# Performance work log

Hardware: AMD Instinct MI355X
Metric: run time of the kernel (lower is better)

Reference implementation:

```python
import jax, jax.numpy as jnp
import numpy as np

B, S, H, NH = 2, 2048, 1024, 16
HD = H // NH  # 64
SCALE = HD ** -0.5


def setup_inputs() -> dict:
    key = jax.random.key(0)
    k1, k2, k3 = jax.random.split(key, 3)
    x = jax.random.normal(k1, (B, S, H), dtype=jnp.float32)
    w_qkv = jax.random.normal(k2, (H, 3 * H), dtype=jnp.float32) * (H ** -0.5)
    b_qkv = jnp.zeros((3 * H,), dtype=jnp.float32)
    w_out = jax.random.normal(k3, (H, H), dtype=jnp.float32) * (H ** -0.5)
    b_out = jnp.zeros((H,), dtype=jnp.float32)
    return {"x": x, "w_qkv": w_qkv, "b_qkv": b_qkv, "w_out": w_out, "b_out": b_out}


def reference(x, w_qkv, b_qkv, w_out, b_out):
    # qkv projection: [B,S,3H] -> split -> [B,NH,S,HD] each
    qkv = x @ w_qkv + b_qkv
    q, k, v = jnp.split(qkv, 3, axis=-1)
    def heads(t):
        return t.reshape(B, S, NH, HD).transpose(0, 2, 1, 3)  # [B,NH,S,HD]
    q, k, v = heads(q), heads(k), heads(v)
    # full (non-causal) softmax attention; chunking in the original is
    # math-equivalent since each query row attends over all keys
    scores = jnp.einsum('bhqd,bhkd->bhqk', q, k) * SCALE
    attn = jax.nn.softmax(scores, axis=-1)
    out = jnp.einsum('bhqk,bhkd->bhqd', attn, v)  # [B,NH,S,HD]
    out = out.transpose(0, 2, 1, 3).reshape(B, S, H)
    # to_out linear (Dropout is identity in eval mode)
    return out @ w_out + b_out
```

## Files before the change

### kernel.cpp

```cpp
#include <hip/hip_runtime.h>
#include <cstdint>

using u16 = unsigned short;
typedef __bf16 bf16x8 __attribute__((ext_vector_type(8)));
typedef __bf16 bf16x4 __attribute__((ext_vector_type(4)));
typedef __bf16 bf16x2 __attribute__((ext_vector_type(2)));
typedef float f32x4 __attribute__((ext_vector_type(4)));

#define MFMA16(a, b, c) __builtin_amdgcn_mfma_f32_16x16x32_bf16((a), (b), (c), 0, 0, 0)

__device__ __forceinline__ u16 f2bf(float f) {
  union { float f; uint32_t u; } c; c.f = f;
  uint32_t u = c.u;
  u += 0x7fffu + ((u >> 16) & 1u);
  return (u16)(u >> 16);
}

#if __has_builtin(__builtin_amdgcn_global_load_lds)
#define GLOAD_LDS16(g, l)                                                      \
  __builtin_amdgcn_global_load_lds(                                            \
      (__attribute__((address_space(1))) void*)(g),                            \
      (__attribute__((address_space(3))) void*)(l), 16, 0, 0)
#else
#define GLOAD_LDS16(g, l) do { *(uint4*)(l) = *(const uint4*)(g); } while (0)
#endif

__device__ __forceinline__ bf16x8 ptrans(const f32x4 lo, const f32x4 hi) {
  union W { bf16x2 h; uint32_t u; } wl0, wl1, wh0, wh1;
  wl0.h[0] = (__bf16)lo[0]; wl0.h[1] = (__bf16)lo[1];
  wl1.h[0] = (__bf16)lo[2]; wl1.h[1] = (__bf16)lo[3];
  wh0.h[0] = (__bf16)hi[0]; wh0.h[1] = (__bf16)hi[1];
  wh1.h[0] = (__bf16)hi[2]; wh1.h[1] = (__bf16)hi[3];
  uint32_t a0 = wl0.u, b0 = wh0.u, a1 = wl1.u, b1 = wh1.u;
  asm("v_permlane32_swap_b32 %0, %1" : "+v"(a0), "+v"(b0));
  asm("v_permlane16_swap_b32 %0, %1" : "+v"(a0), "+v"(b0));
  asm("v_permlane32_swap_b32 %0, %1" : "+v"(a1), "+v"(b1));
  asm("v_permlane16_swap_b32 %0, %1" : "+v"(a1), "+v"(b1));
  union R { uint32_t u[4]; bf16x8 v; } r;
  r.u[0] = a0; r.u[1] = a1; r.u[2] = b0; r.u[3] = b1;
  return r.v;
}

__global__ __launch_bounds__(256) void prep(
    const float* __restrict__ x, const float* __restrict__ w_qkv,
    const float* __restrict__ w_out, u16* __restrict__ xb,
    u16* __restrict__ wqT, u16* __restrict__ woT) {
  const int bid = blockIdx.x, tid = threadIdx.x;
  if (bid < 4096) {
    int i = (bid * 256 + tid) * 4;
    float4 v = *(const float4*)&x[i];
    ushort4 p;
    p.x = f2bf(v.x); p.y = f2bf(v.y); p.z = f2bf(v.z); p.w = f2bf(v.w);
    *(ushort4*)&xb[i] = p;
    return;
  }
  __shared__ float tile[32][33];
  int t = bid - 4096;
  const float* in;
  u16* outp;
  int C, bx, by;
  if (t < 3072) { in = w_qkv; outp = wqT; C = 3072; bx = (t % 96) * 32; by = (t / 96) * 32; }
  else { t -= 3072; in = w_out; outp = woT; C = 1024; bx = (t % 32) * 32; by = (t / 32) * 32; }
  const int tx = tid & 31, ty = tid >> 5;
#pragma unroll
  for (int r2 = 0; r2 < 4; ++r2)
    tile[ty + r2 * 8][tx] = in[(size_t)(by + ty + r2 * 8) * C + bx + tx];
  __syncthreads();
#pragma unroll
  for (int r2 = 0; r2 < 4; ++r2)
    outp[(size_t)(bx + ty + r2 * 8) * 1024 + by + tx] = f2bf(tile[tx][ty + r2 * 8]);
}

__global__ __launch_bounds__(256, 3) void gemm_qkv(
    const u16* __restrict__ A, const u16* __restrict__ Bt,
    const float* __restrict__ bias,
    u16* __restrict__ qb, u16* __restrict__ kb, u16* __restrict__ vb,
    int M, int N, int K) {
  __shared__ u16 As[128 * 32];
  __shared__ u16 Bs[128 * 32];
  const int tid = threadIdx.x;
  const int m0 = blockIdx.x * 128;
  const int n0 = blockIdx.y * 128;
  const int lane = tid & 63, w = tid >> 6;
  const int quad = lane >> 4, l16 = lane & 15;
  const int wr = w >> 1, wc = w & 1;

  f32x4 acc[4][4] = {};

  const int r0 = tid >> 2, p0 = tid & 3;
  const int r1 = r0 + 64;
  const int c8 = p0 ^ ((r0 >> 1) & 3);
  const u16* ga0 = A + (size_t)(m0 + r0) * K + c8 * 8;
  const u16* ga1 = A + (size_t)(m0 + r1) * K + c8 * 8;
  const u16* gb0 = Bt + (size_t)(n0 + r0) * K + c8 * 8;
  const u16* gb1 = Bt + (size_t)(n0 + r1) * K + c8 * 8;
  u16* la0 = &As[tid * 8];
  u16* la1 = &As[(tid + 256) * 8];
  u16* lb0 = &Bs[tid * 8];
  u16* lb1 = &Bs[(tid + 256) * 8];

  int aoff[4], boff[4];
#pragma unroll
  for (int i = 0; i < 4; ++i) {
    int ra = wr * 64 + i * 16 + l16;
    aoff[i] = (ra * 4 + (quad ^ ((ra >> 1) & 3))) * 8;
    int rb = wc * 64 + i * 16 + l16;
    boff[i] = (rb * 4 + (quad ^ ((rb >> 1) & 3))) * 8;
  }

  const int nIter = K >> 5;
  for (int kt = 0; kt < nIter; ++kt) {
    __syncthreads();
    const int kk = kt << 5;
    GLOAD_LDS16(ga0 + kk, la0);
    GLOAD_LDS16(ga1 + kk, la1);
    GLOAD_LDS16(gb0 + kk, lb0);
    GLOAD_LDS16(gb1 + kk, lb1);
    __syncthreads();
    bf16x8 af[4], bfr[4];
#pragma unroll
    for (int i = 0; i < 4; ++i) af[i] = *(const bf16x8*)&As[aoff[i]];
#pragma unroll
    for (int j = 0; j < 4; ++j) bfr[j] = *(const bf16x8*)&Bs[boff[j]];
#pragma unroll
    for (int i = 0; i < 4; ++i)
#pragma unroll
      for (int j = 0; j < 4; ++j)
        acc[i][j] = MFMA16(af[i], bfr[j], acc[i][j]);
  }

  const int S = 2048, NH = 16;
#pragma unroll
  for (int i = 0; i < 4; ++i) {
    const int mb = m0 + wr * 64 + i * 16 + quad * 4;
#pragma unroll
    for (int j = 0; j < 4; ++j) {
      const int n = n0 + wc * 64 + j * 16 + l16;
      const float bv = bias[n];
      const int which = n >> 10;
      const int hn = n & 1023;
      const int h = hn >> 6, d = hn & 63;
      const int b = mb >> 11, s = mb & 2047;
      const int bh = b * NH + h;
      if (which == 2) {
        ushort4 pk;
        pk.x = f2bf(acc[i][j][0] + bv);
        pk.y = f2bf(acc[i][j][1] + bv);
        pk.z = f2bf(acc[i][j][2] + bv);
        pk.w = f2bf(acc[i][j][3] + bv);
        *(ushort4*)&vb[((size_t)bh * 64 + d) * S + s] = pk;
      } else {
        const float sc = (which == 0) ? 0.18033688f : 1.0f;
        u16* dst = (which == 0) ? qb : kb;
#pragma unroll
        for (int r = 0; r < 4; ++r)
          dst[((size_t)bh * S + s + r) * 64 + d] = f2bf((acc[i][j][r] + bv) * sc);
      }
    }
  }
}

__global__ __launch_bounds__(256, 2) void gemm_out(
    const u16* __restrict__ A, const u16* __restrict__ Bt,
    const float* __restrict__ bias, float* __restrict__ outf,
    int M, int N, int K) {
  __shared__ u16 As[64 * 32];
  __shared__ u16 Bs[128 * 32];
  const int tid = threadIdx.x;
  const int m0 = blockIdx.x * 64;
  const int n0 = blockIdx.y * 128;
  const int lane = tid & 63, w = tid >> 6;
  const int quad = lane >> 4, l16 = lane & 15;
  const int wr = w >> 1, wc = w & 1;

  f32x4 acc[2][4] = {};

  const int r0 = tid >> 2, p0 = tid & 3;
  const int c8 = p0 ^ ((r0 >> 1) & 3);
  const u16* ga0 = A + (size_t)(m0 + r0) * K + c8 * 8;
  const u16* gb0 = Bt + (size_t)(n0 + r0) * K + c8 * 8;
  const u16* gb1 = Bt + (size_t)(n0 + r0 + 64) * K + c8 * 8;
  u16* la0 = &As[tid * 8];
  u16* lb0 = &Bs[tid * 8];
  u16* lb1 = &Bs[(tid + 256) * 8];

  int aoff[2], boff[4];
#pragma unroll
  for (int i = 0; i < 2; ++i) {
    int ra = wr * 32 + i * 16 + l16;
    aoff[i] = (ra * 4 + (quad ^ ((ra >> 1) & 3))) * 8;
  }
#pragma unroll
  for (int j = 0; j < 4; ++j) {
    int rb = wc * 64 + j * 16 + l16;
    boff[j] = (rb * 4 + (quad ^ ((rb >> 1) & 3))) * 8;
  }

  const int nIter = K >> 5;
  for (int kt = 0; kt < nIter; ++kt) {
    __syncthreads();
    const int kk = kt << 5;
    GLOAD_LDS16(ga0 + kk, la0);
    GLOAD_LDS16(gb0 + kk, lb0);
    GLOAD_LDS16(gb1 + kk, lb1);
    __syncthreads();
    bf16x8 af[2], bfr[4];
#pragma unroll
    for (int i = 0; i < 2; ++i) af[i] = *(const bf16x8*)&As[aoff[i]];
#pragma unroll
    for (int j = 0; j < 4; ++j) bfr[j] = *(const bf16x8*)&Bs[boff[j]];
#pragma unroll
    for (int i = 0; i < 2; ++i)
#pragma unroll
      for (int j = 0; j < 4; ++j)
        acc[i][j] = MFMA16(af[i], bfr[j], acc[i][j]);
  }

#pragma unroll
  for (int i = 0; i < 2; ++i) {
    const int mb = m0 + wr * 32 + i * 16 + quad * 4;
#pragma unroll
    for (int j = 0; j < 4; ++j) {
      const int n = n0 + wc * 64 + j * 16 + l16;
      const float bv = bias[n];
#pragma unroll
      for (int r = 0; r < 4; ++r)
        outf[(size_t)(mb + r) * N + n] = acc[i][j][r] + bv;
    }
  }
}

__global__ __launch_bounds__(256, 2) void attn_fa(
    const u16* __restrict__ qg, const u16* __restrict__ kg,
    const u16* __restrict__ vg, u16* __restrict__ o) {
  const int S = 2048;
  const int lin = blockIdx.x;
  const int xcd = lin & 7, chunk = lin >> 3;
  const int bh = xcd * 4 + (chunk & 3);
  const int qblk = chunk >> 2;
  const int b = bh >> 4, h = bh & 15;
  const int tid = threadIdx.x, w = tid >> 6, lane = tid & 63;
  const int quad = lane >> 4, l16 = lane & 15;
  const int wq = w >> 1, wk = w & 1;

  __shared__ u16 Ks[2][8192];
  __shared__ u16 Vs[2][8192];

  const int q0w = qblk * 128 + wq * 64;
  bf16x8 qf[4][2];
#pragma unroll
  for (int qt = 0; qt < 4; ++qt)
#pragma unroll
    for (int dh = 0; dh < 2; ++dh)
      qf[qt][dh] = *(const bf16x8*)(qg + ((size_t)bh * S + q0w + qt * 16 + l16) * 64 +
                                    dh * 32 + quad * 8);

  f32x4 accO[4][4] = {};
  f32x4 accL[4] = {};

  bf16x8 ones;
#pragma unroll
  for (int i = 0; i < 8; ++i) ones[i] = (__bf16)1.0f;

  const u16* kbase = kg + (size_t)bh * S * 64;
  const u16* vbase = vg + (size_t)bh * 64 * S;

  const int sr0 = tid >> 3, sp0 = tid & 7;
  const int c8s = sp0 ^ (sr0 & 7);
  const u16* kSrc = kbase + (size_t)sr0 * 64 + c8s * 8;
  const u16* vSrc = vbase + (size_t)sr0 * S + c8s * 8;

  const int kgA = (quad ^ (l16 & 7)) * 8;
  const int kgB = ((quad + 4) ^ (l16 & 7)) * 8;

#define STAGE_KV(KT, NB)                                                      \
  {                                                                           \
    _Pragma("unroll")                                                         \
    for (int seg = 0; seg < 4; ++seg) {                                       \
      GLOAD_LDS16(kSrc + (size_t)((KT) * 128 + seg * 32) * 64,                \
                  &Ks[NB][(seg * 256 + tid) * 8]);                            \
      GLOAD_LDS16(vSrc + (size_t)(seg & 1) * 32 * S + (KT) * 128 +            \
                      (seg >> 1) * 64,                                        \
                  &Vs[NB][(seg * 256 + tid) * 8]);                            \
    }                                                                         \
  }

  STAGE_KV(0, 0);

  for (int kt = 0; kt < 16; ++kt) {
    const int cur = kt & 1;
    __syncthreads();
    const u16* Kc = Ks[cur];
    const u16* Vc = Vs[cur];

    bf16x8 kf[4][2];
#pragma unroll
    for (int ct = 0; ct < 4; ++ct) {
      const int rb = (wk * 64 + ct * 16 + l16) * 64;
      kf[ct][0] = *(const bf16x8*)&Kc[rb + kgA];
      kf[ct][1] = *(const bf16x8*)&Kc[rb + kgB];
    }

    if (kt + 1 < 16) STAGE_KV(kt + 1, cur ^ 1);

    f32x4 s[4][4] = {};
    __builtin_amdgcn_s_setprio(1);
#pragma unroll
    for (int ct = 0; ct < 4; ++ct)
#pragma unroll
      for (int qt = 0; qt < 4; ++qt) {
        s[ct][qt] = MFMA16(kf[ct][0], qf[qt][0], s[ct][qt]);
        s[ct][qt] = MFMA16(kf[ct][1], qf[qt][1], s[ct][qt]);
      }
    __builtin_amdgcn_s_setprio(0);

#pragma unroll
    for (int ct = 0; ct < 4; ++ct)
#pragma unroll
      for (int qt = 0; qt < 4; ++qt)
#pragma unroll
        for (int r = 0; r < 4; ++r)
          s[ct][qt][r] = __builtin_amdgcn_exp2f(s[ct][qt][r]);

    bf16x8 pf[2][4];
#pragma unroll
    for (int qt = 0; qt < 4; ++qt) {
      pf[0][qt] = ptrans(s[0][qt], s[1][qt]);
      pf[1][qt] = ptrans(s[2][qt], s[3][qt]);
    }

    bf16x8 vf[4][2];
#pragma unroll
    for (int dt = 0; dt < 4; ++dt) {
      const int rb = wk * 4096 + (dt * 16 + l16) * 64;
      vf[dt][0] = *(const bf16x8*)&Vc[rb + kgA];
      vf[dt][1] = *(const bf16x8*)&Vc[rb + kgB];
    }

    __builtin_amdgcn_s_setprio(1);
#pragma unroll
    for (int qt = 0; qt < 4; ++qt) {
      accL[qt] = MFMA16(ones, pf[0][qt], accL[qt]);
      accL[qt] = MFMA16(ones, pf[1][qt], accL[qt]);
    }
#pragma unroll
    for (int dt = 0; dt < 4; ++dt)
#pragma unroll
      for (int qt = 0; qt < 4; ++qt) {
        accO[dt][qt] = MFMA16(vf[dt][0], pf[0][qt], accO[dt][qt]);
        accO[dt][qt] = MFMA16(vf[dt][1], pf[1][qt], accO[dt][qt]);
      }
    __builtin_amdgcn_s_setprio(0);
  }
#undef STAGE_KV

  __syncthreads();
  float* redO = (float*)&Ks[0][0];
  float* redL = (float*)&Vs[0][0];
  if (wk == 1) {
#pragma unroll
    for (int dt = 0; dt < 4; ++dt)
#pragma unroll
      for (int qt = 0; qt < 4; ++qt)
        *(f32x4*)&redO[((wq * 16 + dt * 4 + qt) << 8) + lane * 4] = accO[dt][qt];
    if (quad == 0) {
#pragma unroll
      for (int qt = 0; qt < 4; ++qt)
        redL[wq * 64 + qt * 16 + l16] = accL[qt][0];
    }
  }
  __syncthreads();
  if (wk == 0) {
#pragma unroll
    for (int dt = 0; dt < 4; ++dt)
#pragma unroll
      for (int qt = 0; qt < 4; ++qt)
        accO[dt][qt] += *(const f32x4*)&redO[((wq * 16 + dt * 4 + qt) << 8) + lane * 4];
#pragma unroll
    for (int qt = 0; qt < 4; ++qt) {
      const float inv = 1.f / (accL[qt][0] + redL[wq * 64 + qt * 16 + l16]);
      const int qrow = q0w + qt * 16 + l16;
#pragma unroll
      for (int dt = 0; dt < 4; ++dt) {
        ushort4 pk;
        pk.x = f2bf(accO[dt][qt][0] * inv);
        pk.y = f2bf(accO[dt][qt][1] * inv);
        pk.z = f2bf(accO[dt][qt][2] * inv);
        pk.w = f2bf(accO[dt][qt][3] * inv);
        *(ushort4*)&o[(size_t)(b * S + qrow) * 1024 + h * 64 + dt * 16 + quad * 4] = pk;
      }
    }
  }
}


extern "C" void kernel_launch(void* const* d_in, const int* in_sizes, int n_in,
                              void* d_out, int out_size, void* d_ws, size_t ws_size,
                              hipStream_t stream) {
  const float* x = (const float*)d_in[0];
  const float* w_qkv = (const float*)d_in[1];
  const float* b_qkv = (const float*)d_in[2];
  const float* w_out = (const float*)d_in[3];
  const float* b_out = (const float*)d_in[4];
  float* out = (float*)d_out;

  u16* xb = (u16*)d_ws;
  u16* wqT = xb + 4096 * 1024;
  u16* woT = wqT + 3072 * 1024;
  u16* qb = woT + 1024 * 1024;
  u16* kb = qb + 4194304;
  u16* vb = kb + 4194304;
  u16* ao = vb + 4194304;

  prep<<<8192, 256, 0, stream>>>(x, w_qkv, w_out, xb, wqT, woT);
  gemm_qkv<<<dim3(32, 24), 256, 0, stream>>>(xb, wqT, b_qkv, qb, kb, vb,
                                             4096, 3072, 1024);
  attn_fa<<<512, 256, 0, stream>>>(qb, kb, vb, ao);
  gemm_out<<<dim3(64, 8), 256, 0, stream>>>(ao, woT, b_out, out,
                                            4096, 1024, 1024);
}
```

Baseline: 175.5 us.

## Halve attention query tile, load K fragments directly from global, remap QKV GEMM blocks per XCD

The attention kernel now gives each block 64 query rows instead of 128 and launches twice as many blocks with a higher occupancy target. K tiles are no longer staged through shared memory; each wave reads its K fragments straight from global memory, so only V stays double-buffered in LDS. This halves LDS use per block and cuts register pressure, at the cost of more global and L2 traffic for K and less reuse of each K/V tile. The QKV GEMM also remaps its block index so that blocks on the same XCD share M tiles, aiming at better L2 locality.

```diff
diff --git a/kernel.cpp b/kernel.cpp
--- a/kernel.cpp
+++ b/kernel.cpp
@@ -79,8 +79,12 @@
   __shared__ u16 As[128 * 32];
   __shared__ u16 Bs[128 * 32];
   const int tid = threadIdx.x;
-  const int m0 = blockIdx.x * 128;
-  const int n0 = blockIdx.y * 128;
+  const int lin = blockIdx.y * 32 + blockIdx.x;
+  const int xcd = lin & 7;
+  const int r = lin >> 3;
+  const int mi = r & 3, nj = r >> 2;
+  const int m0 = (xcd * 4 + mi) * 128;
+  const int n0 = nj * 128;
   const int lane = tid & 63, w = tid >> 6;
   const int quad = lane >> 4, l16 = lane & 15;
   const int wr = w >> 1, wc = w & 1;
@@ -153,8 +157,8 @@
         const float sc = (which == 0) ? 0.18033688f : 1.0f;
         u16* dst = (which == 0) ? qb : kb;
 #pragma unroll
-        for (int r = 0; r < 4; ++r)
-          dst[((size_t)bh * S + s + r) * 64 + d] = f2bf((acc[i][j][r] + bv) * sc);
+        for (int r2 = 0; r2 < 4; ++r2)
+          dst[((size_t)bh * S + s + r2) * 64 + d] = f2bf((acc[i][j][r2] + bv) * sc);
       }
     }
   }
@@ -230,7 +234,7 @@
   }
 }
 
-__global__ __launch_bounds__(256, 2) void attn_fa(
+__global__ __launch_bounds__(256, 4) void attn_fa(
     const u16* __restrict__ qg, const u16* __restrict__ kg,
     const u16* __restrict__ vg, u16* __restrict__ o) {
   const int S = 2048;
@@ -243,20 +247,19 @@
   const int quad = lane >> 4, l16 = lane & 15;
   const int wq = w >> 1, wk = w & 1;
 
-  __shared__ u16 Ks[2][8192];
   __shared__ u16 Vs[2][8192];
 
-  const int q0w = qblk * 128 + wq * 64;
-  bf16x8 qf[4][2];
-#pragma unroll
-  for (int qt = 0; qt < 4; ++qt)
+  const int q0w = qblk * 64 + wq * 32;
+  bf16x8 qf[2][2];
+#pragma unroll
+  for (int qt = 0; qt < 2; ++qt)
 #pragma unroll
     for (int dh = 0; dh < 2; ++dh)
       qf[qt][dh] = *(const bf16x8*)(qg + ((size_t)bh * S + q0w + qt * 16 + l16) * 64 +
                                     dh * 32 + quad * 8);
 
-  f32x4 accO[4][4] = {};
-  f32x4 accL[4] = {};
+  f32x4 accO[4][2] = {};
+  f32x4 accL[2] = {};
 
   bf16x8 ones;
 #pragma unroll
@@ -265,108 +268,103 @@
   const u16* kbase = kg + (size_t)bh * S * 64;
   const u16* vbase = vg + (size_t)bh * 64 * S;
 
-  const int sr0 = tid >> 3, sp0 = tid & 7;
-  const int c8s = sp0 ^ (sr0 & 7);
-  const u16* kSrc = kbase + (size_t)sr0 * 64 + c8s * 8;
-  const u16* vSrc = vbase + (size_t)sr0 * S + c8s * 8;
+  const u16* kFrag = kbase + (size_t)(wk * 64 + l16) * 64 + quad * 8;
+
+  const int vd0 = tid >> 3, vg0 = tid & 7;
+  const u16* vSrc = vbase + (size_t)vd0 * S + (vg0 ^ (vd0 & 7)) * 8;
 
   const int kgA = (quad ^ (l16 & 7)) * 8;
   const int kgB = ((quad + 4) ^ (l16 & 7)) * 8;
 
-#define STAGE_KV(KT, NB)                                                      \
+#define STAGE_V(KT, NB)                                                       \
   {                                                                           \
     _Pragma("unroll")                                                         \
-    for (int seg = 0; seg < 4; ++seg) {                                       \
-      GLOAD_LDS16(kSrc + (size_t)((KT) * 128 + seg * 32) * 64,                \
-                  &Ks[NB][(seg * 256 + tid) * 8]);                            \
+    for (int seg = 0; seg < 4; ++seg)                                         \
       GLOAD_LDS16(vSrc + (size_t)(seg & 1) * 32 * S + (KT) * 128 +            \
                       (seg >> 1) * 64,                                        \
                   &Vs[NB][(seg * 256 + tid) * 8]);                            \
-    }                                                                         \
-  }
-
-  STAGE_KV(0, 0);
+  }
+
+  STAGE_V(0, 0);
 
   for (int kt = 0; kt < 16; ++kt) {
     const int cur = kt & 1;
     __syncthreads();
-    const u16* Kc = Ks[cur];
-    const u16* Vc = Vs[cur];
-
-    bf16x8 kf[4][2];
+    if (kt + 1 < 16) STAGE_V(kt + 1, cur ^ 1);
+
+    const u16* kT = kFrag + (size_t)kt * 8192;
+    bf16x8 kfA[4], kfB[4];
 #pragma unroll
     for (int ct = 0; ct < 4; ++ct) {
-      const int rb = (wk * 64 + ct * 16 + l16) * 64;
-      kf[ct][0] = *(const bf16x8*)&Kc[rb + kgA];
-      kf[ct][1] = *(const bf16x8*)&Kc[rb + kgB];
-    }
-
-    if (kt + 1 < 16) STAGE_KV(kt + 1, cur ^ 1);
-
-    f32x4 s[4][4] = {};
+      kfA[ct] = *(const bf16x8*)(kT + ct * 1024);
+      kfB[ct] = *(const bf16x8*)(kT + ct * 1024 + 32);
+    }
+
+    f32x4 s[4][2] = {};
     __builtin_amdgcn_s_setprio(1);
 #pragma unroll
     for (int ct = 0; ct < 4; ++ct)
 #pragma unroll
-      for (int qt = 0; qt < 4; ++qt) {
-        s[ct][qt] = MFMA16(kf[ct][0], qf[qt][0], s[ct][qt]);
-        s[ct][qt] = MFMA16(kf[ct][1], qf[qt][1], s[ct][qt]);
+      for (int qt = 0; qt < 2; ++qt) {
+        s[ct][qt] = MFMA16(kfA[ct], qf[qt][0], s[ct][qt]);
+        s[ct][qt] = MFMA16(kfB[ct], qf[qt][1], s[ct][qt]);
       }
     __builtin_amdgcn_s_setprio(0);
 
 #pragma unroll
     for (int ct = 0; ct < 4; ++ct)
 #pragma unroll
-      for (int qt = 0; qt < 4; ++qt)
+      for (int qt = 0; qt < 2; ++qt)
 #pragma unroll
         for (int r = 0; r < 4; ++r)
           s[ct][qt][r] = __builtin_amdgcn_exp2f(s[ct][qt][r]);
 
-    bf16x8 pf[2][4];
-#pragma unroll
-    for (int qt = 0; qt < 4; ++qt) {
+    bf16x8 pf[2][2];
+#pragma unroll
+    for (int qt = 0; qt < 2; ++qt) {
       pf[0][qt] = ptrans(s[0][qt], s[1][qt]);
       pf[1][qt] = ptrans(s[2][qt], s[3][qt]);
     }
 
-    bf16x8 vf[4][2];
+    const u16* Vc = Vs[cur];
+    bf16x8 vfA[4], vfB[4];
 #pragma unroll
     for (int dt = 0; dt < 4; ++dt) {
       const int rb = wk * 4096 + (dt * 16 + l16) * 64;
-      vf[dt][0] = *(const bf16x8*)&Vc[rb + kgA];
-      vf[dt][1] = *(const bf16x8*)&Vc[rb + kgB];
+      vfA[dt] = *(const bf16x8*)&Vc[rb + kgA];
+      vfB[dt] = *(const bf16x8*)&Vc[rb + kgB];
     }
 
     __builtin_amdgcn_s_setprio(1);
 #pragma unroll
-    for (int qt = 0; qt < 4; ++qt) {
+    for (int qt = 0; qt < 2; ++qt) {
       accL[qt] = MFMA16(ones, pf[0][qt], accL[qt]);
       accL[qt] = MFMA16(ones, pf[1][qt], accL[qt]);
     }
 #pragma unroll
     for (int dt = 0; dt < 4; ++dt)
 #pragma unroll
-      for (int qt = 0; qt < 4; ++qt) {
-        accO[dt][qt] = MFMA16(vf[dt][0], pf[0][qt], accO[dt][qt]);
-        accO[dt][qt] = MFMA16(vf[dt][1], pf[1][qt], accO[dt][qt]);
+      for (int qt = 0; qt < 2; ++qt) {
+        accO[dt][qt] = MFMA16(vfA[dt], pf[0][qt], accO[dt][qt]);
+        accO[dt][qt] = MFMA16(vfB[dt], pf[1][qt], accO[dt][qt]);
       }
     __builtin_amdgcn_s_setprio(0);
   }
-#undef STAGE_KV
+#undef STAGE_V
 
   __syncthreads();
-  float* redO = (float*)&Ks[0][0];
-  float* redL = (float*)&Vs[0][0];
+  float* redO = (float*)&Vs[0][0];
+  float* redL = (float*)&Vs[1][0];
   if (wk == 1) {
 #pragma unroll
     for (int dt = 0; dt < 4; ++dt)
 #pragma unroll
-      for (int qt = 0; qt < 4; ++qt)
-        *(f32x4*)&redO[((wq * 16 + dt * 4 + qt) << 8) + lane * 4] = accO[dt][qt];
+      for (int qt = 0; qt < 2; ++qt)
+        *(f32x4*)&redO[((wq * 8 + dt * 2 + qt) << 8) + lane * 4] = accO[dt][qt];
     if (quad == 0) {
 #pragma unroll
-      for (int qt = 0; qt < 4; ++qt)
-        redL[wq * 64 + qt * 16 + l16] = accL[qt][0];
+      for (int qt = 0; qt < 2; ++qt)
+        redL[wq * 32 + qt * 16 + l16] = accL[qt][0];
     }
   }
   __syncthreads();
@@ -374,11 +372,11 @@
 #pragma unroll
     for (int dt = 0; dt < 4; ++dt)
 #pragma unroll
-      for (int qt = 0; qt < 4; ++qt)
-        accO[dt][qt] += *(const f32x4*)&redO[((wq * 16 + dt * 4 + qt) << 8) + lane * 4];
-#pragma unroll
-    for (int qt = 0; qt < 4; ++qt) {
-      const float inv = 1.f / (accL[qt][0] + redL[wq * 64 + qt * 16 + l16]);
+      for (int qt = 0; qt < 2; ++qt)
+        accO[dt][qt] += *(const f32x4*)&redO[((wq * 8 + dt * 2 + qt) << 8) + lane * 4];
+#pragma unroll
+    for (int qt = 0; qt < 2; ++qt) {
+      const float inv = 1.f / (accL[qt][0] + redL[wq * 32 + qt * 16 + l16]);
       const int qrow = q0w + qt * 16 + l16;
 #pragma unroll
       for (int dt = 0; dt < 4; ++dt) {
@@ -415,7 +413,7 @@
   prep<<<8192, 256, 0, stream>>>(x, w_qkv, w_out, xb, wqT, woT);
   gemm_qkv<<<dim3(32, 24), 256, 0, stream>>>(xb, wqT, b_qkv, qb, kb, vb,
                                              4096, 3072, 1024);
-  attn_fa<<<512, 256, 0, stream>>>(qb, kb, vb, ao);
+  attn_fa<<<1024, 256, 0, stream>>>(qb, kb, vb, ao);
   gemm_out<<<dim3(64, 8), 256, 0, stream>>>(ao, woT, b_out, out,
                                             4096, 1024, 1024);
 }
```

After: 209.6 us. +19.4%, slower.
